# Kernel tuning notes

Hardware: AMD Instinct MI355X
Metric: run time of the kernel (lower is better)

Reference implementation:

```python
import jax, jax.numpy as jnp
import numpy as np

EPS = 1e-5
N_LAYERS = 4  # int(log2(patch_size=16))


def _conv(x, w, stride=1, pad=0):
    return jax.lax.conv_general_dilated(
        x, w, (stride, stride), ((pad, pad), (pad, pad)),
        dimension_numbers=('NCHW', 'OIHW', 'NCHW'))


def _mbn(x, m, g, b):
    # masked BatchNorm1d over active (nnz) sites only; m is [B,1,H,W] 0/1
    cnt = jnp.maximum(m.sum(), 1.0)
    mean = (x * m).sum((0, 2, 3)) / cnt
    xc = x - mean[None, :, None, None]
    var = (xc * xc * m).sum((0, 2, 3)) / cnt
    y = xc * jax.lax.rsqrt(var + EPS)[None, :, None, None]
    return (y * g[None, :, None, None] + b[None, :, None, None]) * m


def _down_mask(m):
    # active-output sites of a k=3, stride=2, pad=1 regular sparse conv
    return jax.lax.reduce_window(m, 0.0, jax.lax.max, (1, 1, 3, 3), (1, 1, 2, 2),
                                 ((0, 0), (0, 0), (1, 1), (1, 1)))


def setup_inputs() -> dict:
    key = jax.random.key(0)
    ks = jax.random.split(key, 24)
    B, C, H, W = 8, 3, 256, 256
    hd, ed, L = 192, 192, 256
    w = lambda k, shp: jax.random.normal(k, shp, jnp.float32) * 0.05
    inp = {
        'images': jax.random.normal(ks[0], (B, C, H, W), jnp.float32),
        'mask': jax.random.randint(ks[1], (B, L), 0, 2).astype(jnp.int32),
        'stem_w': w(ks[2], (hd, C, 1, 1)),
        'stem_g': jnp.ones((hd,), jnp.float32), 'stem_b': jnp.zeros((hd,), jnp.float32),
        'dw1': w(ks[3], (N_LAYERS, hd, hd, 3, 3)),
        'dg1': jnp.ones((N_LAYERS, hd), jnp.float32), 'db1': jnp.zeros((N_LAYERS, hd), jnp.float32),
        'dw2': w(ks[4], (N_LAYERS, hd, hd, 3, 3)),
        'dg2': jnp.ones((N_LAYERS, hd), jnp.float32), 'db2': jnp.zeros((N_LAYERS, hd), jnp.float32),
        'rw1': w(ks[5], (N_LAYERS, hd, hd, 3, 3)),
        'rg1': jnp.ones((N_LAYERS, hd), jnp.float32), 'rb1': jnp.zeros((N_LAYERS, hd), jnp.float32),
        'rw2': w(ks[6], (N_LAYERS, hd, hd, 3, 3)),
        'rg2': jnp.ones((N_LAYERS, hd), jnp.float32), 'rb2': jnp.zeros((N_LAYERS, hd), jnp.float32),
        'final_w': w(ks[7], (ed, hd, 1, 1)),
        'final_g': jnp.ones((ed,), jnp.float32), 'final_b': jnp.zeros((ed,), jnp.float32),
    }
    return inp


def reference(images, mask, stem_w, stem_g, stem_b,
              dw1, dg1, db1, dw2, dg2, db2,
              rw1, rg1, rb1, rw2, rg2, rb2,
              final_w, final_g, final_b):
    B, C, H, W = images.shape
    L = mask.shape[1]
    f = int(np.sqrt(L))
    s = H // f
    keep = (1 - mask).astype(images.dtype).reshape(B, f, f)
    m = jnp.repeat(jnp.repeat(keep, s, axis=1), s, axis=2)[:, None]  # [B,1,H,W]
    x = images * m  # dense emulation of sparse tensor: inactive sites are zero

    # stem (regular 1x1 conv, active set unchanged) + BN + ReLU
    x = jnp.maximum(_mbn(_conv(x, stem_w), m, stem_g, stem_b), 0.0)

    for i in range(N_LAYERS):
        # ResBlockDownSparse: regular conv k3 s2 -> BN -> ReLU -> subm conv -> BN
        x = _conv(x, dw1[i], stride=2, pad=1)
        m = _down_mask(m)
        x = jnp.maximum(_mbn(x, m, dg1[i], db1[i]), 0.0)
        x = _mbn(_conv(x, dw2[i], 1, 1), m, dg2[i], db2[i])
        # ResBlockSparse (in==out, no skip projection)
        idn = x
        h = jnp.maximum(_mbn(_conv(x, rw1[i], 1, 1), m, rg1[i], rb1[i]), 0.0)
        h = _mbn(_conv(h, rw2[i], 1, 1), m, rg2[i], rb2[i])
        x = jnp.maximum(h + idn, 0.0)

    # final 1x1 subm proj + BN + ReLU
    x = jnp.maximum(_mbn(_conv(x, final_w), m, final_g, final_b), 0.0)
    ids_restore = jnp.tile(jnp.arange(L, dtype=jnp.int32)[None], (B, 1))
    return x, mask, ids_restore
```

## Files before the change

### kernel.cpp

```cpp
#include <hip/hip_runtime.h>
#include <hip/hip_bf16.h>

typedef __hip_bfloat16 bf16;
typedef unsigned short u16;
typedef unsigned int u32;
typedef unsigned char u8;
typedef __attribute__((ext_vector_type(8))) short bf16x8;
typedef __attribute__((ext_vector_type(4))) float f32x4;

#define NB 8
#define CH 192
#define WSZ (CH*CH*9)


static __device__ __forceinline__ float bf2f(bf16 v){ return __bfloat162float(v); }
static __device__ __forceinline__ u16 f2bu(float f){
  union { bf16 h; u16 u; } cv; cv.h = __float2bfloat16(f); return cv.u;
}
static __device__ __forceinline__ float u2f(u16 u){
  union { bf16 h; u16 u; } cv; cv.u = u; return __bfloat162float(cv.h);
}
static __device__ __forceinline__ u32 pk2bf(float a, float b){
  union { __hip_bfloat162 h; u32 u; } cv;
  cv.h = __float22bfloat162_rn(make_float2(a, b));
  return cv.u;
}

static __device__ __forceinline__ void build_ss(const float* __restrict__ stIn,
        const float* __restrict__ g, const float* __restrict__ bb,
        const float* __restrict__ cnt, float* scs, float* shs, int t){
  if(t < CH){
    float s = 0.f, s2 = 0.f;
#pragma unroll
    for(int b=0;b<NB;b++){ s += stIn[b*384 + t]; s2 += stIn[b*384 + 192 + t]; }
    float n = fmaxf(*cnt, 1.0f);
    float mean = s/n;
    float var = fmaxf(s2/n - mean*mean, 0.f);
    float rstd = rsqrtf(var + 1e-5f);
    float sc = g[t]*rstd;
    scs[t] = sc;
    shs[t] = bb[t] - mean*sc;
  }
}

template<int RELU>
static __device__ __forceinline__ uint4 affine8(uint4 v, const float* scp, const float* shp){
  float4 sa = *(const float4*)(scp);
  float4 sb = *(const float4*)(scp+4);
  float4 ha = *(const float4*)(shp);
  float4 hb = *(const float4*)(shp+4);
  u16* pv = (u16*)&v;
  float f0, f1;
  f0 = u2f(pv[0])*sa.x + ha.x; f1 = u2f(pv[1])*sa.y + ha.y;
  if(RELU){ f0 = fmaxf(f0,0.f); f1 = fmaxf(f1,0.f); }
  ((u32*)&v)[0] = pk2bf(f0, f1);
  f0 = u2f(pv[2])*sa.z + ha.z; f1 = u2f(pv[3])*sa.w + ha.w;
  if(RELU){ f0 = fmaxf(f0,0.f); f1 = fmaxf(f1,0.f); }
  ((u32*)&v)[1] = pk2bf(f0, f1);
  f0 = u2f(pv[4])*sb.x + hb.x; f1 = u2f(pv[5])*sb.y + hb.y;
  if(RELU){ f0 = fmaxf(f0,0.f); f1 = fmaxf(f1,0.f); }
  ((u32*)&v)[2] = pk2bf(f0, f1);
  f0 = u2f(pv[6])*sb.z + hb.z; f1 = u2f(pv[7])*sb.w + hb.w;
  if(RELU){ f0 = fmaxf(f0,0.f); f1 = fmaxf(f1,0.f); }
  ((u32*)&v)[3] = pk2bf(f0, f1);
  return v;
}


__global__ void k_zero(float* p, int n){
  int i = blockIdx.x*blockDim.x + threadIdx.x;
  if(i < n) p[i] = 0.f;
}

__global__ void k_fill(float* p, int n, float v){
  int i = blockIdx.x*blockDim.x + threadIdx.x;
  if(i < n) p[i] = v;
}

__global__ void k_mask0(const int* __restrict__ mask, u8* __restrict__ m0){
  int i = blockIdx.x*blockDim.x + threadIdx.x;
  if(i >= NB*65536) return;
  int b = i >> 16; int p = i & 65535;
  int y = p >> 8, x = p & 255;
  int patch = (y >> 4)*16 + (x >> 4);
  m0[i] = (u8)(1 - mask[b*256 + patch]);
}

__global__ void k_maskdown(const u8* __restrict__ mi, u8* __restrict__ mo,
                           int Ho, int Wo, int Hi, int Wi){
  int i = blockIdx.x*blockDim.x + threadIdx.x;
  int total = NB*Ho*Wo; if(i >= total) return;
  int b = i/(Ho*Wo); int p = i%(Ho*Wo);
  int oy = p/Wo, ox = p%Wo;
  u8 v = 0;
  for(int ky=0; ky<3; ky++){
    int iy = oy*2 + ky - 1; if(iy < 0 || iy >= Hi) continue;
    for(int kx=0; kx<3; kx++){
      int ix = ox*2 + kx - 1; if(ix < 0 || ix >= Wi) continue;
      u8 t = mi[(b*Hi + iy)*Wi + ix]; if(t > v) v = t;
    }
  }
  mo[i] = v;
}

__global__ void k_count(const u8* __restrict__ m, int n, float* cnt){
  int i = blockIdx.x*blockDim.x + threadIdx.x;
  int stride = gridDim.x*blockDim.x;
  int local = 0;
  for(int j=i; j<n; j+=stride) local += m[j];
  for(int o=32; o>0; o>>=1) local += __shfl_down(local, o, 64);
  if((threadIdx.x & 63) == 0 && local) atomicAdd(cnt, (float)local);
}


__global__ __launch_bounds__(256) void k_moments(const float* __restrict__ im,
        const u8* __restrict__ m0, float* __restrict__ mom){
  float s[9];
#pragma unroll
  for(int k=0;k<9;k++) s[k]=0.f;
  int stride = gridDim.x*blockDim.x;
  for(int i = blockIdx.x*blockDim.x + threadIdx.x; i < NB*65536; i += stride){
    if(m0[i]){
      int b = i >> 16, p = i & 65535;
      float r = im[(size_t)(b*3+0)*65536 + p];
      float g = im[(size_t)(b*3+1)*65536 + p];
      float bl= im[(size_t)(b*3+2)*65536 + p];
      s[0]+=r;    s[1]+=g;    s[2]+=bl;
      s[3]+=r*r;  s[4]+=g*g;  s[5]+=bl*bl;
      s[6]+=r*g;  s[7]+=r*bl; s[8]+=g*bl;
    }
  }
#pragma unroll
  for(int k=0;k<9;k++){
    for(int o=32; o>0; o>>=1) s[k] += __shfl_down(s[k], o, 64);
  }
  __shared__ float sh[4][9];
  int w = threadIdx.x >> 6;
  if((threadIdx.x & 63) == 0){
#pragma unroll
    for(int k=0;k<9;k++) sh[w][k] = s[k];
  }
  __syncthreads();
  if(threadIdx.x < 9){
    float tt = sh[0][threadIdx.x] + sh[1][threadIdx.x] + sh[2][threadIdx.x] + sh[3][threadIdx.x];
    atomicAdd(&mom[threadIdx.x], tt);
  }
}

__global__ void k_stemfinal(const float* __restrict__ mom, const float* __restrict__ cnt,
        const float* __restrict__ sw, const float* __restrict__ g,
        const float* __restrict__ bb, float* __restrict__ ssA){
  int c = threadIdx.x; if(c >= CH) return;
  float n = fmaxf(*cnt, 1.0f);
  float m0=mom[0], m1=mom[1], m2=mom[2], m3=mom[3], m4=mom[4];
  float m5=mom[5], m6=mom[6], m7=mom[7], m8=mom[8];
  float w0 = sw[c*3+0], w1 = sw[c*3+1], w2 = sw[c*3+2];
  float mean = (w0*m0 + w1*m1 + w2*m2)/n;
  float e2 = (w0*w0*m3 + w1*w1*m4 + w2*w2*m5
            + 2.f*(w0*w1*m6 + w0*w2*m7 + w1*w2*m8))/n;
  float var = fmaxf(e2 - mean*mean, 0.f);
  float sc = g[c]*rsqrtf(var + 1e-5f);
  ssA[c] = sc;
  ssA[CH + c] = bb[c] - mean*sc;
}

__global__ void k_fold(const float* __restrict__ sw, const float* __restrict__ ssA,
                       float* __restrict__ swf){
  int c = threadIdx.x; if(c >= CH) return;
  float sc = ssA[c];
  swf[c*4+0] = sc*sw[c*3+0];
  swf[c*4+1] = sc*sw[c*3+1];
  swf[c*4+2] = sc*sw[c*3+2];
  swf[c*4+3] = ssA[CH+c];
}

__global__ void k_repack16(const float* __restrict__ dw1, const float* __restrict__ dw2,
                           const float* __restrict__ rw1, const float* __restrict__ rw2,
                           bf16* __restrict__ wb){
  int i = blockIdx.x*blockDim.x + threadIdx.x;
  if(i >= 16*WSZ) return;
  int stage = i/(4*WSZ);
  int sel = (i/WSZ)%4;
  int r = i%WSZ;
  const float* w = (sel==0)?dw1 : (sel==1)?dw2 : (sel==2)?rw1 : rw2;
  float val = w[(size_t)stage*WSZ + r];
  int tap = r%9; int ci = (r/9)%CH; int co = r/(9*CH);
  wb[(size_t)(stage*4+sel)*WSZ + tap*CH*CH + co*CH + ci] = __float2bfloat16(val);
}

__global__ void k_repackF(const float* __restrict__ fw, bf16* __restrict__ wb){
  int i = blockIdx.x*blockDim.x + threadIdx.x;
  if(i < CH*CH) wb[i] = __float2bfloat16(fw[i]);
}


static __device__ __forceinline__ void epi_stats(f32x4 (&acc)[4][3], const u8* sm,
        float* __restrict__ statsB, int b, int co0, int l15, int q, int lane){
  float s[3], s2[3];
#pragma unroll
  for(int nt=0;nt<3;nt++){ s[nt]=0.f; s2[nt]=0.f; }
#pragma unroll
  for(int mt=0;mt<4;mt++){
#pragma unroll
    for(int r=0;r<4;r++){
      int site = mt*16 + q*4 + r;
      float mv = (float)sm[site];
#pragma unroll
      for(int nt=0;nt<3;nt++){
        float v = acc[mt][nt][r]*mv;
        s[nt] += v; s2[nt] += v*v;
      }
    }
  }
#pragma unroll
  for(int nt=0;nt<3;nt++){
    s[nt]  += __shfl_down(s[nt], 32, 64);  s[nt]  += __shfl_down(s[nt], 16, 64);
    s2[nt] += __shfl_down(s2[nt], 32, 64); s2[nt] += __shfl_down(s2[nt], 16, 64);
  }
  if(lane < 16){
#pragma unroll
    for(int nt=0;nt<3;nt++){
      int co = co0 + nt*16 + l15;
      atomicAdd(&statsB[b*384 + co], s[nt]);
      atomicAdd(&statsB[b*384 + 192 + co], s2[nt]);
    }
  }
}

static __device__ __forceinline__ void epi_store(f32x4 (&acc)[4][3], u16* obuf,
        u16* __restrict__ out, int b, int oy0, int ox0, int Ho, int Wo,
        int t, int co0, int l15, int q){
  __syncthreads();
#pragma unroll
  for(int mt=0;mt<4;mt++){
#pragma unroll
    for(int nt=0;nt<3;nt++){
      int co = co0 + nt*16 + l15;
#pragma unroll
      for(int r=0;r<4;r++){
        int site = mt*16 + q*4 + r;
        obuf[site*212 + co] = f2bu(acc[mt][nt][r]);
      }
    }
  }
  __syncthreads();
  for(int e=t; e<3072; e+=256){
    int r = e/384; int off = (e%384)*4;
    int sx = off/CH, co = off%CH;
    ushort4 v = *(const ushort4*)&obuf[(r*8+sx)*212 + co];
    *(ushort4*)(out + ((size_t)(b*Ho+oy0+r)*Wo + ox0)*CH + off) = v;
  }
}


static __device__ __forceinline__ void epi_stats8(f32x4 (&acc)[8][3], const u8* sm,
        float* __restrict__ statsB, int b, int co0, int l15, int q, int lane){
  float s[3], s2[3];
#pragma unroll
  for(int nt=0;nt<3;nt++){ s[nt]=0.f; s2[nt]=0.f; }
#pragma unroll
  for(int mt=0;mt<8;mt++){
#pragma unroll
    for(int r=0;r<4;r++){
      int site = mt*16 + q*4 + r;
      float mv = (float)sm[site];
#pragma unroll
      for(int nt=0;nt<3;nt++){
        float v = acc[mt][nt][r]*mv;
        s[nt] += v; s2[nt] += v*v;
      }
    }
  }
#pragma unroll
  for(int nt=0;nt<3;nt++){
    s[nt]  += __shfl_down(s[nt], 32, 64);  s[nt]  += __shfl_down(s[nt], 16, 64);
    s2[nt] += __shfl_down(s2[nt], 32, 64); s2[nt] += __shfl_down(s2[nt], 16, 64);
  }
  if(lane < 16){
#pragma unroll
    for(int nt=0;nt<3;nt++){
      int co = co0 + nt*16 + l15;
      atomicAdd(&statsB[b*384 + co], s[nt]);
      atomicAdd(&statsB[b*384 + 192 + co], s2[nt]);
    }
  }
}

static __device__ __forceinline__ void epi_store_q(f32x4 (&acc)[8][3], u16* obuf,
        u16* __restrict__ out, int b, int oy0, int ox0, int Ho, int Wo,
        int t, int co0, int l15, int q, int qd){
  __syncthreads();
#pragma unroll
  for(int mi=0; mi<2; mi++){
    int mt = qd*2 + mi;
#pragma unroll
    for(int nt=0;nt<3;nt++){
      int co = co0 + nt*16 + l15;
#pragma unroll
      for(int r=0;r<4;r++){
        int site = mi*16 + q*4 + r;
        obuf[site*212 + co] = f2bu(acc[mt][nt][r]);
      }
    }
  }
  __syncthreads();
  for(int e=t; e<1536; e+=256){
    int r = e/384; int off = (e%384)*4;
    int sx = off/CH, co = off%CH;
    ushort4 v = *(const ushort4*)&obuf[(r*8+sx)*212 + co];
    *(ushort4*)(out + ((size_t)(b*Ho+oy0+qd*4+r)*Wo + ox0)*CH + off) = v;
  }
}


static __device__ __forceinline__ void epi_statsT(f32x4 (&acc)[2][3], const u8* sm,
        float* __restrict__ statsB, int b, int co0, int l15, int q, int lane, int mh){
  float s[3], s2[3];
#pragma unroll
  for(int nt=0;nt<3;nt++){ s[nt]=0.f; s2[nt]=0.f; }
#pragma unroll
  for(int mt=0;mt<2;mt++){
#pragma unroll
    for(int r=0;r<4;r++){
      int site = mh*32 + mt*16 + q*4 + r;
      float mv = (float)sm[site];
#pragma unroll
      for(int nt=0;nt<3;nt++){
        float v = acc[mt][nt][r]*mv;
        s[nt] += v; s2[nt] += v*v;
      }
    }
  }
#pragma unroll
  for(int nt=0;nt<3;nt++){
    s[nt]  += __shfl_down(s[nt], 32, 64);  s[nt]  += __shfl_down(s[nt], 16, 64);
    s2[nt] += __shfl_down(s2[nt], 32, 64); s2[nt] += __shfl_down(s2[nt], 16, 64);
  }
  if(lane < 16){
#pragma unroll
    for(int nt=0;nt<3;nt++){
      int co = co0 + nt*16 + l15;
      atomicAdd(&statsB[b*384 + co], s[nt]);
      atomicAdd(&statsB[b*384 + 192 + co], s2[nt]);
    }
  }
}

static __device__ __forceinline__ void epi_storeT(f32x4 (&acc)[2][3], u16* obuf,
        u16* __restrict__ out, int b, int oy0, int ox0, int Ho, int Wo,
        int t, int w, int coh, int l15, int q, int mh){
  __syncthreads();
#pragma unroll
  for(int mt=0;mt<2;mt++){
#pragma unroll
    for(int nt=0;nt<3;nt++){
      int col = (w&1)*48 + nt*16 + l15;
#pragma unroll
      for(int r=0;r<4;r++){
        int site = mh*32 + mt*16 + q*4 + r;
        obuf[site*104 + col] = f2bu(acc[mt][nt][r]);
      }
    }
  }
  __syncthreads();
  for(int e=t; e<1536; e+=256){
    int site = e/24; int grp = e%24;
    ushort4 v = *(const ushort4*)&obuf[site*104 + grp*4];
    *(ushort4*)(out + ((size_t)(b*Ho+oy0+(site>>3))*Wo + ox0+(site&7))*CH + coh*96 + grp*4) = v;
  }
}

#define CIP 104
template<int RELU>
__global__ __launch_bounds__(256) void k_convm(const bf16* __restrict__ in,
        const bf16* __restrict__ wb, const u8* __restrict__ mk,
        bf16* __restrict__ out, int Ho, int Wo,
        const float* __restrict__ stIn, const float* __restrict__ gIn,
        const float* __restrict__ bIn, const float* __restrict__ cnt,
        float* __restrict__ statsB){
  __shared__ __align__(16) u16 tile[180*CIP];
  __shared__ __align__(16) float scs[CH], shs[CH];
  __shared__ u8 sm[128];
  __shared__ u8 wmk[180];
  __shared__ int anyact;
  const int t = threadIdx.x;
  const int b = blockIdx.z;
  const int ox0 = blockIdx.x*8, oy0 = blockIdx.y*16;
  const int gy0 = oy0 - 1, gx0 = ox0 - 1;

  if(t == 0) anyact = 0;
  __syncthreads();
  if(t < 128){
    int r = t >> 3, c = t & 7;
    u8 mv = mk[(b*Ho + oy0 + r)*Wo + ox0 + c];
    sm[t] = mv;
    if(mv) anyact = 1;
  }
  for(int e=t; e<180; e+=256){
    int y = e/10, x = e%10;
    int gy = gy0 + y, gx = gx0 + x;
    u8 mv = 0;
    if(gy >= 0 && gy < Ho && gx >= 0 && gx < Wo) mv = mk[(b*Ho+gy)*Wo+gx];
    wmk[e] = mv;
  }
  __syncthreads();
  if(!anyact) return;

  build_ss(stIn, gIn, bIn, cnt, scs, shs, t);
  __syncthreads();

  const u16* inp = (const u16*)in;
  const int w = t >> 6;
  const int l = t & 63;
  const int l15 = l & 15, q = l >> 4;
  f32x4 acc[8][3];
#pragma unroll
  for(int mt=0;mt<8;mt++)
#pragma unroll
    for(int nt=0;nt<3;nt++) acc[mt][nt] = (f32x4){0.f,0.f,0.f,0.f};

  int sy[8], sx[8];
#pragma unroll
  for(int mt=0;mt<8;mt++){ int s = mt*16 + l15; sy[mt] = s>>3; sx[mt] = s&7; }
  const int co0 = w*48;
  const u16* wt = (const u16*)wb;
  int bco[3];
#pragma unroll
  for(int nt=0;nt<3;nt++) bco[nt] = (co0 + nt*16 + l15)*CH + q*8;

  for(int p=0; p<2; p++){
    if(p) __syncthreads();
    const int cb = p*96;
    for(int u=t; u<2160; u+=256){
      int site = u/12; int grp = u%12;
      int y = site/10, x = site%10;
      int gy = gy0 + y, gx = gx0 + x;
      uint4 v = {0u,0u,0u,0u};
      if(wmk[site]){
        v = *(const uint4*)(inp + ((size_t)(b*Ho+gy)*Wo+gx)*CH + cb + grp*8);
        v = affine8<RELU>(v, &scs[cb + grp*8], &shs[cb + grp*8]);
      }
      *(uint4*)&tile[site*CIP + grp*8] = v;
    }
    __syncthreads();
    for(int tap=0; tap<9; tap++){
      const int ky = tap/3, kx = tap%3;
      const u16* tb[8];
#pragma unroll
      for(int mt=0;mt<8;mt++)
        tb[mt] = &tile[((sy[mt]+ky)*10 + sx[mt]+kx)*CIP + q*8];
      const u16* wt0 = wt + (size_t)tap*CH*CH + cb;
#pragma unroll
      for(int c=0;c<3;c++){
        bf16x8 a[8], bb[3];
#pragma unroll
        for(int mt=0;mt<8;mt++) a[mt] = *(const bf16x8*)(tb[mt] + c*32);
#pragma unroll
        for(int nt=0;nt<3;nt++) bb[nt] = *(const bf16x8*)(wt0 + bco[nt] + c*32);
#pragma unroll
        for(int mt=0;mt<8;mt++)
#pragma unroll
          for(int nt=0;nt<3;nt++)
            acc[mt][nt] = __builtin_amdgcn_mfma_f32_16x16x32_bf16(a[mt], bb[nt], acc[mt][nt], 0, 0, 0);
      }
    }
  }
  epi_stats8(acc, sm, statsB, b, co0, l15, q, l);
  epi_store_q(acc, tile, (u16*)out, b, oy0, ox0, Ho, Wo, t, co0, l15, q, 0);
  epi_store_q(acc, tile, (u16*)out, b, oy0, ox0, Ho, Wo, t, co0, l15, q, 1);
  epi_store_q(acc, tile, (u16*)out, b, oy0, ox0, Ho, Wo, t, co0, l15, q, 2);
  epi_store_q(acc, tile, (u16*)out, b, oy0, ox0, Ho, Wo, t, co0, l15, q, 3);
}

#define CIPT 200
template<int RELU>
__global__ __launch_bounds__(256) void k_convmT(const bf16* __restrict__ in,
        const bf16* __restrict__ wb, const u8* __restrict__ mk,
        bf16* __restrict__ out, int Ho, int Wo,
        const float* __restrict__ stIn, const float* __restrict__ gIn,
        const float* __restrict__ bIn, const float* __restrict__ cnt,
        float* __restrict__ statsB){
  __shared__ __align__(16) u16 tile[100*CIPT];
  __shared__ __align__(16) float scs[CH], shs[CH];
  __shared__ u8 sm[64];
  __shared__ u8 wmk[100];
  __shared__ int anyact;
  const int t = threadIdx.x;
  const int zb = blockIdx.z;
  const int b = zb & (NB-1);
  const int coh = zb >> 3;
  const int ox0 = blockIdx.x*8, oy0 = blockIdx.y*8;
  const int gy0 = oy0 - 1, gx0 = ox0 - 1;

  if(t == 0) anyact = 0;
  __syncthreads();
  if(t < 64){
    int r = t >> 3, c = t & 7;
    u8 mv = mk[(b*Ho + oy0 + r)*Wo + ox0 + c];
    sm[t] = mv;
    if(mv) anyact = 1;
  } else if(t < 164){
    int e = t - 64;
    int y = e/10, x = e%10;
    int gy = gy0 + y, gx = gx0 + x;
    u8 mv = 0;
    if(gy >= 0 && gy < Ho && gx >= 0 && gx < Wo) mv = mk[(b*Ho+gy)*Wo+gx];
    wmk[e] = mv;
  }
  __syncthreads();
  if(!anyact) return;

  build_ss(stIn, gIn, bIn, cnt, scs, shs, t);
  __syncthreads();

  const u16* inp = (const u16*)in;
  for(int u=t; u<2400; u+=256){
    int y = u/240; int rem = u%240; int x = rem/24; int cu = rem%24;
    int gy = gy0 + y, gx = gx0 + x;
    uint4 v = {0u,0u,0u,0u};
    if(wmk[y*10+x]){
      v = *(const uint4*)(inp + ((size_t)(b*Ho+gy)*Wo+gx)*CH + cu*8);
      v = affine8<RELU>(v, &scs[cu*8], &shs[cu*8]);
    }
    *(uint4*)&tile[(y*10+x)*CIPT + cu*8] = v;
  }
  __syncthreads();

  const int w = t >> 6;
  const int l = t & 63;
  const int l15 = l & 15, q = l >> 4;
  const int mh = w >> 1;
  f32x4 acc[2][3];
#pragma unroll
  for(int mt=0;mt<2;mt++)
#pragma unroll
    for(int nt=0;nt<3;nt++) acc[mt][nt] = (f32x4){0.f,0.f,0.f,0.f};

  int sy[2], sx[2];
#pragma unroll
  for(int mt=0;mt<2;mt++){ int s = mh*32 + mt*16 + l15; sy[mt] = s>>3; sx[mt] = s&7; }
  const int co0 = coh*96 + (w&1)*48;
  const u16* wt = (const u16*)wb;
  int bco[3];
#pragma unroll
  for(int nt=0;nt<3;nt++) bco[nt] = (co0 + nt*16 + l15)*CH + q*8;

  for(int tap=0; tap<9; tap++){
    const int ky = tap/3, kx = tap%3;
    const u16* tb[2];
#pragma unroll
    for(int mt=0;mt<2;mt++)
      tb[mt] = &tile[((sy[mt]+ky)*10 + sx[mt]+kx)*CIPT + q*8];
    const u16* wt0 = wt + (size_t)tap*CH*CH;
#pragma unroll
    for(int c=0;c<6;c++){
      bf16x8 a[2], bb[3];
#pragma unroll
      for(int mt=0;mt<2;mt++) a[mt] = *(const bf16x8*)(tb[mt] + c*32);
#pragma unroll
      for(int nt=0;nt<3;nt++) bb[nt] = *(const bf16x8*)(wt0 + bco[nt] + c*32);
#pragma unroll
      for(int mt=0;mt<2;mt++)
#pragma unroll
        for(int nt=0;nt<3;nt++)
          acc[mt][nt] = __builtin_amdgcn_mfma_f32_16x16x32_bf16(a[mt], bb[nt], acc[mt][nt], 0, 0, 0);
    }
  }
  epi_statsT(acc, sm, statsB, b, co0, l15, q, l, mh);
  epi_storeT(acc, tile, (u16*)out, b, oy0, ox0, Ho, Wo, t, w, coh, l15, q, mh);
}


__global__ __launch_bounds__(256) void k_convs2T(const bf16* __restrict__ in,
        const bf16* __restrict__ wb, const u8* __restrict__ mk,
        bf16* __restrict__ out, int Ho, int Wo, float* __restrict__ statsB){
  __shared__ __align__(16) u16 obuf[64*104];
  __shared__ u8 sm[64];
  __shared__ int anyact;
  const int t = threadIdx.x;
  const int zb = blockIdx.z;
  const int b = zb & (NB-1);
  const int coh = zb >> 3;
  const int ox0 = blockIdx.x*8, oy0 = blockIdx.y*8;
  const int Hi = Ho*2, Wi = Wo*2;

  if(t == 0) anyact = 0;
  __syncthreads();
  if(t < 64){
    int r = t >> 3, c = t & 7;
    u8 mv = mk[(b*Ho + oy0 + r)*Wo + ox0 + c];
    sm[t] = mv;
    if(mv) anyact = 1;
  }
  __syncthreads();
  if(!anyact) return;

  const u16* inp = (const u16*)in;
  const int w = t >> 6;
  const int l = t & 63;
  const int l15 = l & 15, q = l >> 4;
  const int mh = w >> 1;
  f32x4 acc[2][3];
#pragma unroll
  for(int mt=0;mt<2;mt++)
#pragma unroll
    for(int nt=0;nt<3;nt++) acc[mt][nt] = (f32x4){0.f,0.f,0.f,0.f};

  int gyb[2], gxb[2];
#pragma unroll
  for(int mt=0;mt<2;mt++){
    int s = mh*32 + mt*16 + l15;
    gyb[mt] = (oy0 + (s>>3))*2 - 1;
    gxb[mt] = (ox0 + (s&7))*2 - 1;
  }
  const int co0 = coh*96 + (w&1)*48;
  const bf16x8 zro = {0,0,0,0,0,0,0,0};
  const u16* wt = (const u16*)wb;
  int bco[3];
#pragma unroll
  for(int nt=0;nt<3;nt++) bco[nt] = (co0 + nt*16 + l15)*CH + q*8;

  for(int tap=0; tap<9; tap++){
    const int ky = tap/3, kx = tap%3;
    const u16* ap[2]; bool av[2];
#pragma unroll
    for(int mt=0;mt<2;mt++){
      int gy = gyb[mt] + ky, gx = gxb[mt] + kx;
      av[mt] = (gy >= 0 && gy < Hi && gx >= 0 && gx < Wi);
      ap[mt] = inp + ((size_t)(b*Hi+gy)*Wi+gx)*CH + q*8;
    }
    const u16* wt0 = wt + (size_t)tap*CH*CH;
#pragma unroll
    for(int c=0;c<6;c++){
      bf16x8 a[2], bb[3];
#pragma unroll
      for(int mt=0;mt<2;mt++) a[mt] = av[mt] ? *(const bf16x8*)(ap[mt] + c*32) : zro;
#pragma unroll
      for(int nt=0;nt<3;nt++) bb[nt] = *(const bf16x8*)(wt0 + bco[nt] + c*32);
#pragma unroll
      for(int mt=0;mt<2;mt++)
#pragma unroll
        for(int nt=0;nt<3;nt++)
          acc[mt][nt] = __builtin_amdgcn_mfma_f32_16x16x32_bf16(a[mt], bb[nt], acc[mt][nt], 0, 0, 0);
    }
  }
  epi_statsT(acc, sm, statsB, b, co0, l15, q, l, mh);
  epi_storeT(acc, obuf, (u16*)out, b, oy0, ox0, Ho, Wo, t, w, coh, l15, q, mh);
}

#define CIP0 36
#define NS0 561
__global__ __launch_bounds__(256) void k_conv0m(const float* __restrict__ im,
        const float* __restrict__ swf, const u8* __restrict__ m0,
        const bf16* __restrict__ wb, const u8* __restrict__ mk,
        bf16* __restrict__ out, float* __restrict__ statsB){
  __shared__ __align__(16) u16 tile[NS0*CIP0];
  __shared__ __align__(16) u16 bfr[576*8];
  __shared__ u8 sm[128];
  __shared__ int anyact;
  const int t = threadIdx.x;
  const int b = blockIdx.z;
  const int ox0 = blockIdx.x*8, oy0 = blockIdx.y*16;

  if(t == 0) anyact = 0;
  __syncthreads();
  if(t < 128){
    int r = t >> 3, c = t & 7;
    u8 mv = mk[(b*128 + oy0 + r)*128 + ox0 + c];
    sm[t] = mv;
    if(mv) anyact = 1;
  }
  __syncthreads();
  if(!anyact) return;

  const int gy0 = oy0*2 - 1, gx0 = ox0*2 - 1;
  for(int e=t; e<576; e+=256){
    u32 w0=0u, w1=0u, w2=0u, w3=0u;
    if(e < NS0){
      int y = e/17, x = e%17;
      int gy = gy0 + y, gx = gx0 + x;
      if(gy >= 0 && gy < 256 && gx >= 0 && gx < 256){
        int pi = gy*256 + gx;
        if(m0[b*65536 + pi]){
          float rm = im[(size_t)(b*3+0)*65536 + pi];
          float gm = im[(size_t)(b*3+1)*65536 + pi];
          float bm = im[(size_t)(b*3+2)*65536 + pi];
          float rh = u2f(f2bu(rm)), gh = u2f(f2bu(gm)), bh = u2f(f2bu(bm));
          w0 = pk2bf(rm, gm);      w1 = pk2bf(bm, 1.0f);
          w2 = pk2bf(rm-rh, gm-gh); w3 = pk2bf(bm-bh, 0.f);
        }
      }
    }
    *(uint4*)&bfr[e*8] = make_uint4(w0, w1, w2, w3);
  }

  const int w = t >> 6;
  const int l = t & 63;
  const int l15 = l & 15, q = l >> 4;
  const bf16x8 zf = {0,0,0,0,0,0,0,0};

  f32x4 acc[8][3];
#pragma unroll
  for(int mt=0;mt<8;mt++)
#pragma unroll
    for(int nt=0;nt<3;nt++) acc[mt][nt] = (f32x4){0.f,0.f,0.f,0.f};

  int siy[8], six[8];
#pragma unroll
  for(int mt=0;mt<8;mt++){ int s = mt*16 + l15; siy[mt] = (s>>3)*2; six[mt] = (s&7)*2; }
  const int co0 = w*48;
  const u16* wt = (const u16*)wb;
  int bco[3];
#pragma unroll
  for(int nt=0;nt<3;nt++) bco[nt] = (co0 + nt*16 + l15)*CH + q*8;

  for(int h=0; h<6; h++){
    __syncthreads();
    bf16x8 af[2];
#pragma unroll
    for(int mtl=0;mtl<2;mtl++){
      af[mtl] = zf;
      if(q == 0){
        const float4 wv = *(const float4*)&swf[(h*32 + mtl*16 + l15)*4];
        u32 wlo = pk2bf(wv.x, wv.y);
        ((u32*)&af[mtl])[0] = wlo;
        ((u32*)&af[mtl])[1] = pk2bf(wv.z, wv.w);
        ((u32*)&af[mtl])[2] = wlo;
        ((u32*)&af[mtl])[3] = pk2bf(wv.z, 0.f);
      }
    }
#pragma unroll
    for(int i=0;i<9;i++){
      int nt = w + i*4;
      int site = nt*16 + l15;
      bf16x8 bs = zf;
      if(q == 0) bs = *(const bf16x8*)&bfr[(site < 576 ? site : 575)*8];
#pragma unroll
      for(int mtl=0;mtl<2;mtl++){
        f32x4 d = __builtin_amdgcn_mfma_f32_16x16x32_bf16(af[mtl], bs,
                        (f32x4){0.f,0.f,0.f,0.f}, 0, 0, 0);
        if(site < NS0){
          u32 lo = pk2bf(fmaxf(d[0],0.f), fmaxf(d[1],0.f));
          u32 hi = pk2bf(fmaxf(d[2],0.f), fmaxf(d[3],0.f));
          *(uint2*)&tile[site*CIP0 + mtl*16 + q*4] = make_uint2(lo, hi);
        }
      }
    }
    __syncthreads();
    for(int tap=0; tap<9; tap++){
      const int ky = tap/3, kx = tap%3;
      const u16* wt0 = wt + (size_t)tap*CH*CH + h*32;
      bf16x8 a[8], bb[3];
#pragma unroll
      for(int mt=0;mt<8;mt++)
        a[mt] = *(const bf16x8*)&tile[((siy[mt]+ky)*17 + six[mt]+kx)*CIP0 + q*8];
#pragma unroll
      for(int nt=0;nt<3;nt++) bb[nt] = *(const bf16x8*)(wt0 + bco[nt]);
#pragma unroll
      for(int mt=0;mt<8;mt++)
#pragma unroll
        for(int nt=0;nt<3;nt++)
          acc[mt][nt] = __builtin_amdgcn_mfma_f32_16x16x32_bf16(a[mt], bb[nt], acc[mt][nt], 0, 0, 0);
    }
  }
  epi_stats8(acc, sm, statsB, b, co0, l15, q, l);
  epi_store_q(acc, tile, (u16*)out, b, oy0, ox0, 128, 128, t, co0, l15, q, 0);
  epi_store_q(acc, tile, (u16*)out, b, oy0, ox0, 128, 128, t, co0, l15, q, 1);
  epi_store_q(acc, tile, (u16*)out, b, oy0, ox0, 128, 128, t, co0, l15, q, 2);
  epi_store_q(acc, tile, (u16*)out, b, oy0, ox0, 128, 128, t, co0, l15, q, 3);
}


__global__ __launch_bounds__(256) void k_resid(const bf16* __restrict__ xD,
        const bf16* __restrict__ xB, const u8* __restrict__ m,
        const float* __restrict__ stD, const float* __restrict__ gD, const float* __restrict__ bD,
        const float* __restrict__ stB, const float* __restrict__ gB, const float* __restrict__ bB,
        const float* __restrict__ cnt, bf16* __restrict__ out, int sites){
  __shared__ __align__(16) float scD[CH], shD[CH], scB[CH], shB[CH];
  const int t = threadIdx.x;
  build_ss(stD, gD, bD, cnt, scD, shD, t);
  build_ss(stB, gB, bB, cnt, scB, shB, t);
  __syncthreads();
  int idx = blockIdx.x*256 + t;
  int total = sites*24;
  if(idx >= total) return;
  int si = idx/24; int c0 = (idx%24)*8;
  float mv = (float)m[si];
  const u16* pd = (const u16*)xD + (size_t)si*CH + c0;
  const u16* pb = (const u16*)xB + (size_t)si*CH + c0;
  uint4 vd = *(const uint4*)pd;
  uint4 vb = *(const uint4*)pb;
  u16* dd = (u16*)&vd; u16* db = (u16*)&vb;
  uint4 vo;
#pragma unroll
  for(int j=0;j<4;j++){
    int c = c0 + j*2;
    float f0 = (u2f(dd[j*2  ])*scD[c  ] + shD[c  ])*mv + (u2f(db[j*2  ])*scB[c  ] + shB[c  ])*mv;
    float f1 = (u2f(dd[j*2+1])*scD[c+1] + shD[c+1])*mv + (u2f(db[j*2+1])*scB[c+1] + shB[c+1])*mv;
    ((u32*)&vo)[j] = pk2bf(fmaxf(f0, 0.f), fmaxf(f1, 0.f));
  }
  *(uint4*)((u16*)out + (size_t)si*CH + c0) = vo;
}


__global__ __launch_bounds__(256) void k_finalm(const bf16* __restrict__ in,
        const bf16* __restrict__ wb, const u8* __restrict__ m4,
        bf16* __restrict__ out, float* __restrict__ statsB){
  __shared__ __align__(16) u16 obuf[64*212];
  __shared__ u8 sm[64];
  __shared__ int anyact;
  const int t = threadIdx.x;
  const int b = blockIdx.z;
  const int base = blockIdx.x*64;

  if(t == 0) anyact = 0;
  __syncthreads();
  if(t < 64){
    u8 mv = m4[b*256 + base + t];
    sm[t] = mv;
    if(mv) anyact = 1;
  }
  __syncthreads();
  if(!anyact) return;

  const int w = t >> 6;
  const int l = t & 63;
  const int l15 = l & 15, q = l >> 4;
  const int co0 = w*48;
  f32x4 acc[4][3];
#pragma unroll
  for(int mt=0;mt<4;mt++)
#pragma unroll
    for(int nt=0;nt<3;nt++) acc[mt][nt] = (f32x4){0.f,0.f,0.f,0.f};

  const u16* inp = (const u16*)in + (size_t)(b*256 + base)*CH + q*8;
  const u16* wt0 = (const u16*)wb;
#pragma unroll
  for(int c=0;c<6;c++){
    bf16x8 a[4], bb[3];
#pragma unroll
    for(int mt=0;mt<4;mt++)
      a[mt] = *(const bf16x8*)(inp + (size_t)(mt*16 + l15)*CH + c*32);
#pragma unroll
    for(int nt=0;nt<3;nt++){
      int co = co0 + nt*16 + l15;
      bb[nt] = *(const bf16x8*)(wt0 + co*CH + c*32 + q*8);
    }
#pragma unroll
    for(int mt=0;mt<4;mt++)
#pragma unroll
      for(int nt=0;nt<3;nt++)
        acc[mt][nt] = __builtin_amdgcn_mfma_f32_16x16x32_bf16(a[mt], bb[nt], acc[mt][nt], 0, 0, 0);
  }
  epi_stats(acc, sm, statsB, b, co0, l15, q, l);
  epi_store(acc, obuf, (u16*)out, b, blockIdx.x*8, 0, 32, 8, t, co0, l15, q);
}

__global__ __launch_bounds__(256) void k_bnapply_out(const bf16* __restrict__ x,
        const u8* __restrict__ m, const float* __restrict__ stF,
        const float* __restrict__ g, const float* __restrict__ bb,
        const float* __restrict__ cnt, float* __restrict__ out){
  __shared__ __align__(16) float scs[CH], shs[CH];
  const int t = threadIdx.x;
  build_ss(stF, g, bb, cnt, scs, shs, t);
  __syncthreads();
  int i = blockIdx.x*256 + t;
  if(i >= NB*CH*256) return;
  int p = i % 256; int c = (i/256) % CH; int b = i/(256*CH);
  int si = b*256 + p;
  float v = bf2f(x[(size_t)si*CH + c])*scs[c] + shs[c];
  v *= (float)m[si];
  v = fmaxf(v, 0.f);
  out[i] = v;
}


__global__ void k_tail(const int* __restrict__ mask, float* __restrict__ out){
  int i = blockIdx.x*blockDim.x + threadIdx.x;
  if(i < 2048){
    out[393216 + i] = (float)mask[i];
  } else if(i < 4096){
    int j = i - 2048;
    out[395264 + j] = (float)(j & 255);
  }
}


extern "C" void kernel_launch(void* const* d_in, const int* in_sizes, int n_in,
                              void* d_out, int out_size, void* d_ws, size_t ws_size,
                              hipStream_t stream){
  const float* images = (const float*)d_in[0];
  const int*   maskI  = (const int*)d_in[1];
  const float* stem_w = (const float*)d_in[2];
  const float* stem_g = (const float*)d_in[3];
  const float* stem_b = (const float*)d_in[4];
  const float* dw1 = (const float*)d_in[5];
  const float* dg1 = (const float*)d_in[6];
  const float* db1 = (const float*)d_in[7];
  const float* dw2 = (const float*)d_in[8];
  const float* dg2 = (const float*)d_in[9];
  const float* db2 = (const float*)d_in[10];
  const float* rw1 = (const float*)d_in[11];
  const float* rg1 = (const float*)d_in[12];
  const float* rb1 = (const float*)d_in[13];
  const float* rw2 = (const float*)d_in[14];
  const float* rg2 = (const float*)d_in[15];
  const float* rb2 = (const float*)d_in[16];
  const float* final_w = (const float*)d_in[17];
  const float* final_g = (const float*)d_in[18];
  const float* final_b = (const float*)d_in[19];
  float* outF = (float*)d_out;

  char* wsp = (char*)d_ws;
  auto alloc = [&](size_t bytes)->char*{
    char* p = wsp; wsp += (bytes + 255) & ~(size_t)255; return p;
  };
  bf16* S0 = (bf16*)alloc((size_t)NB*CH*16384*2);
  bf16* S1 = (bf16*)alloc((size_t)NB*CH*16384*2);
  bf16* S2 = (bf16*)alloc((size_t)NB*CH*16384*2);
  int Hs[5] = {256,128,64,32,16};
  u8* M[5];
  for(int l=0;l<5;l++) M[l] = (u8*)alloc((size_t)NB*Hs[l]*Hs[l]);
  bf16*  Wb16 = (bf16*)alloc((size_t)17*WSZ*2);
  float* swf = (float*)alloc(CH*4*4);
  float* statsB16 = (float*)alloc((size_t)17*NB*384*4);
  float* statsF = (float*)alloc(384*4);
  float* ssA   = (float*)alloc(2*CH*4);
  float* cnts  = (float*)alloc(8*4);
  size_t need = (size_t)(wsp - (char*)d_ws);

  if(ws_size < need){
    k_fill<<<(393216+255)/256, 256, 0, stream>>>(outF, 393216, 777.0f);
    k_tail<<<16, 256, 0, stream>>>(maskI, outF);
    return;
  }

  int nz = 17*NB*384 + 384;
  k_zero<<<(nz+255)/256, 256, 0, stream>>>(statsB16, nz);
  k_zero<<<1, 32, 0, stream>>>(cnts, 8);
  k_repack16<<<(16*WSZ+255)/256, 256, 0, stream>>>(dw1, dw2, rw1, rw2, Wb16);
  k_repackF<<<(CH*CH+255)/256, 256, 0, stream>>>(final_w, Wb16 + (size_t)16*WSZ);

  k_mask0<<<(NB*65536+255)/256, 256, 0, stream>>>(maskI, M[0]);
  for(int l=1;l<5;l++){
    int total = NB*Hs[l]*Hs[l];
    k_maskdown<<<(total+255)/256, 256, 0, stream>>>(M[l-1], M[l], Hs[l], Hs[l], Hs[l-1], Hs[l-1]);
  }
  for(int l=0;l<5;l++){
    int n = NB*Hs[l]*Hs[l];
    int blocks = (n + 256*64 - 1)/(256*64); if(blocks < 1) blocks = 1; if(blocks > 256) blocks = 256;
    k_count<<<blocks, 256, 0, stream>>>(M[l], n, cnts + l);
  }

  k_moments<<<512, 256, 0, stream>>>(images, M[0], statsF);
  k_stemfinal<<<1, CH, 0, stream>>>(statsF, cnts + 0, stem_w, stem_g, stem_b, ssA);
  k_fold<<<1, CH, 0, stream>>>(stem_w, ssA, swf);

  bf16* X = nullptr;
  for(int i=0;i<4;i++){
    int Ho = Hs[i+1];
    int sites = NB*Ho*Ho;
    const u8* mk = M[i+1];
    const float* cnt = cnts + i + 1;
    bf16* A = S0;
    bf16* B = (i % 2 == 0) ? S1 : S2;
    bf16* C2 = (i == 0) ? S2 : X;
    const bf16* W0 = Wb16 + (size_t)(i*4+0)*WSZ;
    const bf16* W1 = Wb16 + (size_t)(i*4+1)*WSZ;
    const bf16* W2 = Wb16 + (size_t)(i*4+2)*WSZ;
    const bf16* W3 = Wb16 + (size_t)(i*4+3)*WSZ;
    float* st0 = statsB16 + (size_t)(i*4+0)*NB*384;
    float* st1 = statsB16 + (size_t)(i*4+1)*NB*384;
    float* st2 = statsB16 + (size_t)(i*4+2)*NB*384;
    float* st3 = statsB16 + (size_t)(i*4+3)*NB*384;

    dim3 gT(Ho/8, Ho/8, NB*2);
    if(i == 0){
      k_conv0m<<<dim3(16, 8, NB), 256, 0, stream>>>(images, swf, M[0], W0, M[1], A, st0);
    } else {
      k_convs2T<<<gT, 256, 0, stream>>>(X, W0, mk, A, Ho, Ho, st0);
    }
    if(Ho >= 64){
      dim3 g2(Ho/8, Ho/16, NB);
      k_convm<1><<<g2, 256, 0, stream>>>(A, W1, mk, B, Ho, Ho,
          st0, dg1 + i*CH, db1 + i*CH, cnt, st1);
      k_convm<0><<<g2, 256, 0, stream>>>(B, W2, mk, A, Ho, Ho,
          st1, dg2 + i*CH, db2 + i*CH, cnt, st2);
      k_convm<1><<<g2, 256, 0, stream>>>(A, W3, mk, C2, Ho, Ho,
          st2, rg1 + i*CH, rb1 + i*CH, cnt, st3);
    } else {
      k_convmT<1><<<gT, 256, 0, stream>>>(A, W1, mk, B, Ho, Ho,
          st0, dg1 + i*CH, db1 + i*CH, cnt, st1);
      k_convmT<0><<<gT, 256, 0, stream>>>(B, W2, mk, A, Ho, Ho,
          st1, dg2 + i*CH, db2 + i*CH, cnt, st2);
      k_convmT<1><<<gT, 256, 0, stream>>>(A, W3, mk, C2, Ho, Ho,
          st2, rg1 + i*CH, rb1 + i*CH, cnt, st3);
    }
    k_resid<<<(sites*24 + 255)/256, 256, 0, stream>>>(C2, B, mk,
        st3, rg2 + i*CH, rb2 + i*CH,
        st1, dg2 + i*CH, db2 + i*CH, cnt, B, sites);
    X = B;
  }

  float* stF = statsB16 + (size_t)16*NB*384;
  k_finalm<<<dim3(4, 1, NB), 256, 0, stream>>>(X, Wb16 + (size_t)16*WSZ, M[4], S0, stF);
  k_bnapply_out<<<(NB*CH*256 + 255)/256, 256, 0, stream>>>(S0, M[4], stF,
      final_g, final_b, cnts + 4, outF);

  k_tail<<<16, 256, 0, stream>>>(maskI, outF);
}
```

Before: 1.246 ms.

## Block weight layout by 32-channel chunks and prefetch second input half

Weights are repacked so each 32-input-channel chunk for all output channels is contiguous. Each MFMA B-fragment load then reads a compact 64-byte row per lane instead of striding by the full channel count, which should improve cache-line use for every conv kernel. In the main 3x3 conv, the second 96-channel half of the input tile is prefetched into registers before the first half's compute and written to shared memory afterwards, overlapping global latency with MFMA work. The prefetch costs extra VGPRs, which may lower occupancy.

```diff
diff --git a/kernel.cpp b/kernel.cpp
--- a/kernel.cpp
+++ b/kernel.cpp
@@ -11,6 +11,7 @@
 #define NB 8
 #define CH 192
 #define WSZ (CH*CH*9)
+#define WBLK (CH*32)
 
 
 static __device__ __forceinline__ float bf2f(bf16 v){ return __bfloat162float(v); }
@@ -185,12 +186,15 @@
   const float* w = (sel==0)?dw1 : (sel==1)?dw2 : (sel==2)?rw1 : rw2;
   float val = w[(size_t)stage*WSZ + r];
   int tap = r%9; int ci = (r/9)%CH; int co = r/(9*CH);
-  wb[(size_t)(stage*4+sel)*WSZ + tap*CH*CH + co*CH + ci] = __float2bfloat16(val);
+  wb[(size_t)(stage*4+sel)*WSZ + ((size_t)(tap*6 + (ci>>5))*CH + co)*32 + (ci&31)]
+      = __float2bfloat16(val);
 }
 
 __global__ void k_repackF(const float* __restrict__ fw, bf16* __restrict__ wb){
   int i = blockIdx.x*blockDim.x + threadIdx.x;
-  if(i < CH*CH) wb[i] = __float2bfloat16(fw[i]);
+  if(i >= CH*CH) return;
+  int co = i/CH, ci = i%CH;
+  wb[((size_t)(ci>>5)*CH + co)*32 + (ci&31)] = __float2bfloat16(fw[i]);
 }
 
 
@@ -426,45 +430,83 @@
   const u16* wt = (const u16*)wb;
   int bco[3];
 #pragma unroll
-  for(int nt=0;nt<3;nt++) bco[nt] = (co0 + nt*16 + l15)*CH + q*8;
-
-  for(int p=0; p<2; p++){
-    if(p) __syncthreads();
-    const int cb = p*96;
-    for(int u=t; u<2160; u+=256){
-      int site = u/12; int grp = u%12;
-      int y = site/10, x = site%10;
-      int gy = gy0 + y, gx = gx0 + x;
-      uint4 v = {0u,0u,0u,0u};
-      if(wmk[site]){
-        v = *(const uint4*)(inp + ((size_t)(b*Ho+gy)*Wo+gx)*CH + cb + grp*8);
-        v = affine8<RELU>(v, &scs[cb + grp*8], &shs[cb + grp*8]);
-      }
-      *(uint4*)&tile[site*CIP + grp*8] = v;
-    }
-    __syncthreads();
+  for(int nt=0;nt<3;nt++) bco[nt] = (co0 + nt*16 + l15)*32 + q*8;
+
+  auto compute = [&](int cb3){
     for(int tap=0; tap<9; tap++){
       const int ky = tap/3, kx = tap%3;
       const u16* tb[8];
 #pragma unroll
       for(int mt=0;mt<8;mt++)
         tb[mt] = &tile[((sy[mt]+ky)*10 + sx[mt]+kx)*CIP + q*8];
-      const u16* wt0 = wt + (size_t)tap*CH*CH + cb;
 #pragma unroll
       for(int c=0;c<3;c++){
-        bf16x8 a[8], bb[3];
+        const u16* wp = wt + (size_t)(tap*6 + cb3 + c)*WBLK;
+        bf16x8 a[8], bbv[3];
 #pragma unroll
         for(int mt=0;mt<8;mt++) a[mt] = *(const bf16x8*)(tb[mt] + c*32);
 #pragma unroll
-        for(int nt=0;nt<3;nt++) bb[nt] = *(const bf16x8*)(wt0 + bco[nt] + c*32);
+        for(int nt=0;nt<3;nt++) bbv[nt] = *(const bf16x8*)(wp + bco[nt]);
 #pragma unroll
         for(int mt=0;mt<8;mt++)
 #pragma unroll
           for(int nt=0;nt<3;nt++)
-            acc[mt][nt] = __builtin_amdgcn_mfma_f32_16x16x32_bf16(a[mt], bb[nt], acc[mt][nt], 0, 0, 0);
+            acc[mt][nt] = __builtin_amdgcn_mfma_f32_16x16x32_bf16(a[mt], bbv[nt], acc[mt][nt], 0, 0, 0);
       }
     }
-  }
+  };
+
+  for(int u=t; u<2160; u+=256){
+    int site = u/12; int grp = u%12;
+    int y = site/10, x = site%10;
+    int gy = gy0 + y, gx = gx0 + x;
+    uint4 v = {0u,0u,0u,0u};
+    if(wmk[site]){
+      v = *(const uint4*)(inp + ((size_t)(b*Ho+gy)*Wo+gx)*CH + grp*8);
+      v = affine8<RELU>(v, &scs[grp*8], &shs[grp*8]);
+    }
+    *(uint4*)&tile[site*CIP + grp*8] = v;
+  }
+  __syncthreads();
+
+  uint4 pf[8];
+#pragma unroll
+  for(int i=0;i<8;i++){
+    int u = t + i*256;
+    int site = u/12; int grp = u%12;
+    pf[i] = (uint4){0u,0u,0u,0u};
+    if(wmk[site]){
+      int y = site/10, x = site%10;
+      pf[i] = *(const uint4*)(inp + ((size_t)(b*Ho+gy0+y)*Wo+gx0+x)*CH + 96 + grp*8);
+    }
+  }
+
+  compute(0);
+  __syncthreads();
+
+#pragma unroll
+  for(int i=0;i<8;i++){
+    int u = t + i*256;
+    int site = u/12; int grp = u%12;
+    uint4 v = {0u,0u,0u,0u};
+    if(wmk[site]) v = affine8<RELU>(pf[i], &scs[96 + grp*8], &shs[96 + grp*8]);
+    *(uint4*)&tile[site*CIP + grp*8] = v;
+  }
+  if(t < 112){
+    int u = 2048 + t;
+    int site = u/12; int grp = u%12;
+    uint4 v = {0u,0u,0u,0u};
+    if(wmk[site]){
+      int y = site/10, x = site%10;
+      v = *(const uint4*)(inp + ((size_t)(b*Ho+gy0+y)*Wo+gx0+x)*CH + 96 + grp*8);
+      v = affine8<RELU>(v, &scs[96 + grp*8], &shs[96 + grp*8]);
+    }
+    *(uint4*)&tile[site*CIP + grp*8] = v;
+  }
+  __syncthreads();
+
+  compute(3);
+
   epi_stats8(acc, sm, statsB, b, co0, l15, q, l);
   epi_store_q(acc, tile, (u16*)out, b, oy0, ox0, Ho, Wo, t, co0, l15, q, 0);
   epi_store_q(acc, tile, (u16*)out, b, oy0, ox0, Ho, Wo, t, co0, l15, q, 1);
@@ -543,7 +585,7 @@
   const u16* wt = (const u16*)wb;
   int bco[3];
 #pragma unroll
-  for(int nt=0;nt<3;nt++) bco[nt] = (co0 + nt*16 + l15)*CH + q*8;
+  for(int nt=0;nt<3;nt++) bco[nt] = (co0 + nt*16 + l15)*32 + q*8;
 
   for(int tap=0; tap<9; tap++){
     const int ky = tap/3, kx = tap%3;
@@ -551,19 +593,19 @@
 #pragma unroll
     for(int mt=0;mt<2;mt++)
       tb[mt] = &tile[((sy[mt]+ky)*10 + sx[mt]+kx)*CIPT + q*8];
-    const u16* wt0 = wt + (size_t)tap*CH*CH;
 #pragma unroll
     for(int c=0;c<6;c++){
-      bf16x8 a[2], bb[3];
+      const u16* wp = wt + (size_t)(tap*6 + c)*WBLK;
+      bf16x8 a[2], bbv[3];
 #pragma unroll
       for(int mt=0;mt<2;mt++) a[mt] = *(const bf16x8*)(tb[mt] + c*32);
 #pragma unroll
-      for(int nt=0;nt<3;nt++) bb[nt] = *(const bf16x8*)(wt0 + bco[nt] + c*32);
+      for(int nt=0;nt<3;nt++) bbv[nt] = *(const bf16x8*)(wp + bco[nt]);
 #pragma unroll
       for(int mt=0;mt<2;mt++)
 #pragma unroll
         for(int nt=0;nt<3;nt++)
-          acc[mt][nt] = __builtin_amdgcn_mfma_f32_16x16x32_bf16(a[mt], bb[nt], acc[mt][nt], 0, 0, 0);
+          acc[mt][nt] = __builtin_amdgcn_mfma_f32_16x16x32_bf16(a[mt], bbv[nt], acc[mt][nt], 0, 0, 0);
     }
   }
   epi_statsT(acc, sm, statsB, b, co0, l15, q, l, mh);
@@ -618,7 +660,7 @@
   const u16* wt = (const u16*)wb;
   int bco[3];
 #pragma unroll
-  for(int nt=0;nt<3;nt++) bco[nt] = (co0 + nt*16 + l15)*CH + q*8;
+  for(int nt=0;nt<3;nt++) bco[nt] = (co0 + nt*16 + l15)*32 + q*8;
 
   for(int tap=0; tap<9; tap++){
     const int ky = tap/3, kx = tap%3;
@@ -629,19 +671,19 @@
       av[mt] = (gy >= 0 && gy < Hi && gx >= 0 && gx < Wi);
       ap[mt] = inp + ((size_t)(b*Hi+gy)*Wi+gx)*CH + q*8;
     }
-    const u16* wt0 = wt + (size_t)tap*CH*CH;
 #pragma unroll
     for(int c=0;c<6;c++){
-      bf16x8 a[2], bb[3];
+      const u16* wp = wt + (size_t)(tap*6 + c)*WBLK;
+      bf16x8 a[2], bbv[3];
 #pragma unroll
       for(int mt=0;mt<2;mt++) a[mt] = av[mt] ? *(const bf16x8*)(ap[mt] + c*32) : zro;
 #pragma unroll
-      for(int nt=0;nt<3;nt++) bb[nt] = *(const bf16x8*)(wt0 + bco[nt] + c*32);
+      for(int nt=0;nt<3;nt++) bbv[nt] = *(const bf16x8*)(wp + bco[nt]);
 #pragma unroll
       for(int mt=0;mt<2;mt++)
 #pragma unroll
         for(int nt=0;nt<3;nt++)
-          acc[mt][nt] = __builtin_amdgcn_mfma_f32_16x16x32_bf16(a[mt], bb[nt], acc[mt][nt], 0, 0, 0);
+          acc[mt][nt] = __builtin_amdgcn_mfma_f32_16x16x32_bf16(a[mt], bbv[nt], acc[mt][nt], 0, 0, 0);
     }
   }
   epi_statsT(acc, sm, statsB, b, co0, l15, q, l, mh);
@@ -712,7 +754,7 @@
   const u16* wt = (const u16*)wb;
   int bco[3];
 #pragma unroll
-  for(int nt=0;nt<3;nt++) bco[nt] = (co0 + nt*16 + l15)*CH + q*8;
+  for(int nt=0;nt<3;nt++) bco[nt] = (co0 + nt*16 + l15)*32 + q*8;
 
   for(int h=0; h<6; h++){
     __syncthreads();
@@ -749,18 +791,18 @@
     __syncthreads();
     for(int tap=0; tap<9; tap++){
       const int ky = tap/3, kx = tap%3;
-      const u16* wt0 = wt + (size_t)tap*CH*CH + h*32;
-      bf16x8 a[8], bb[3];
+      const u16* wp = wt + (size_t)(tap*6 + h)*WBLK;
+      bf16x8 a[8], bbv[3];
 #pragma unroll
       for(int mt=0;mt<8;mt++)
         a[mt] = *(const bf16x8*)&tile[((siy[mt]+ky)*17 + six[mt]+kx)*CIP0 + q*8];
 #pragma unroll
-      for(int nt=0;nt<3;nt++) bb[nt] = *(const bf16x8*)(wt0 + bco[nt]);
+      for(int nt=0;nt<3;nt++) bbv[nt] = *(const bf16x8*)(wp + bco[nt]);
 #pragma unroll
       for(int mt=0;mt<8;mt++)
 #pragma unroll
         for(int nt=0;nt<3;nt++)
-          acc[mt][nt] = __builtin_amdgcn_mfma_f32_16x16x32_bf16(a[mt], bb[nt], acc[mt][nt], 0, 0, 0);
+          acc[mt][nt] = __builtin_amdgcn_mfma_f32_16x16x32_bf16(a[mt], bbv[nt], acc[mt][nt], 0, 0, 0);
     }
   }
   epi_stats8(acc, sm, statsB, b, co0, l15, q, l);
@@ -834,23 +876,24 @@
     for(int nt=0;nt<3;nt++) acc[mt][nt] = (f32x4){0.f,0.f,0.f,0.f};
 
   const u16* inp = (const u16*)in + (size_t)(b*256 + base)*CH + q*8;
-  const u16* wt0 = (const u16*)wb;
+  const u16* wt = (const u16*)wb;
+  int bco[3];
+#pragma unroll
+  for(int nt=0;nt<3;nt++) bco[nt] = (co0 + nt*16 + l15)*32 + q*8;
 #pragma unroll
   for(int c=0;c<6;c++){
-    bf16x8 a[4], bb[3];
+    const u16* wp = wt + (size_t)c*WBLK;
+    bf16x8 a[4], bbv[3];
 #pragma unroll
     for(int mt=0;mt<4;mt++)
       a[mt] = *(const bf16x8*)(inp + (size_t)(mt*16 + l15)*CH + c*32);
 #pragma unroll
-    for(int nt=0;nt<3;nt++){
-      int co = co0 + nt*16 + l15;
-      bb[nt] = *(const bf16x8*)(wt0 + co*CH + c*32 + q*8);
-    }
+    for(int nt=0;nt<3;nt++) bbv[nt] = *(const bf16x8*)(wp + bco[nt]);
 #pragma unroll
     for(int mt=0;mt<4;mt++)
 #pragma unroll
       for(int nt=0;nt<3;nt++)
-        acc[mt][nt] = __builtin_amdgcn_mfma_f32_16x16x32_bf16(a[mt], bb[nt], acc[mt][nt], 0, 0, 0);
+        acc[mt][nt] = __builtin_amdgcn_mfma_f32_16x16x32_bf16(a[mt], bbv[nt], acc[mt][nt], 0, 0, 0);
   }
   epi_stats(acc, sm, statsB, b, co0, l15, q, l);
   epi_store(acc, obuf, (u16*)out, b, blockIdx.x*8, 0, 32, 8, t, co0, l15, q);
```

Result: no change. 1.241 ms (-0.4%).
